# Performance work log

Hardware: AMD Instinct MI355X
Metric: run time of the kernel (lower is better)

Reference implementation:

```python
import jax, jax.numpy as jnp
import numpy as np

S, B, V, E, H, C, NV = 256, 64, 50000, 300, 512, 46, 4
EPS = 1e-8


def setup_inputs() -> dict:
    key = jax.random.key(0)
    ks = jax.random.split(key, 17)
    f = lambda i, shape, s=0.05: jax.random.normal(ks[i], shape, jnp.float32) * s
    return {
        "seq": jax.random.randint(ks[0], (S, B), 0, V),
        "emb_table": f(1, (V, E), 1.0),
        "w_ih0": f(2, (4 * H, E)), "w_hh0": f(3, (4 * H, H)),
        "b_ih0": f(4, (4 * H,)), "b_hh0": f(5, (4 * H,)),
        "w_ih1": f(6, (4 * H, H)), "w_hh1": f(7, (4 * H, H)),
        "b_ih1": f(8, (4 * H,)), "b_hh1": f(9, (4 * H,)),
        "lin_w": f(10, (H, H)), "lin_b": f(11, (H,)),
        "out_w": f(12, (C, H)), "out_b": f(13, (C,)),
        "pred_w": f(14, (C, 2 * C)), "pred_b": f(15, (C,)),
        "label_embed": f(16, (C, NV, E), 1.0),
    }


def _lstm_layer(x, w_ih, w_hh, b_ih, b_hh):
    # x: [S, B, in]; PyTorch gate order i, f, g, o
    bsz, hid = x.shape[1], w_hh.shape[1]

    def step(carry, xt):
        h, c = carry
        g = xt @ w_ih.T + h @ w_hh.T + b_ih + b_hh  # [B, 4H]
        i, fg, gg, o = jnp.split(g, 4, axis=-1)
        c = jax.nn.sigmoid(fg) * c + jax.nn.sigmoid(i) * jnp.tanh(gg)
        h = jax.nn.sigmoid(o) * jnp.tanh(c)
        return (h, c), h

    h0 = jnp.zeros((bsz, hid), x.dtype)
    _, hs = jax.lax.scan(step, (h0, h0), x)
    return hs  # [S, B, H]


def reference(seq, emb_table, w_ih0, w_hh0, b_ih0, b_hh0, w_ih1, w_hh1, b_ih1, b_hh1,
              lin_w, lin_b, out_w, out_b, pred_w, pred_b, label_embed):
    embed = emb_table[seq]  # [S, B, E]
    h = _lstm_layer(embed, w_ih0, w_hh0, b_ih0, b_hh0)
    h = _lstm_layer(h, w_ih1, w_hh1, b_ih1, b_hh1)  # dropout inactive (eval)
    feature = h[-1] @ lin_w.T + lin_b               # [B, H]
    lstm_output = feature @ out_w.T + out_b         # [B, C]

    # Batched replacement of the per-label/value cosine-similarity loop:
    # cos[s,b,c,v] = <embed[s,b], label[c,v]> / max(|embed[s,b]|*|label[c,v]|, eps)
    en = jnp.linalg.norm(embed, axis=-1)            # [S, B]
    ln = jnp.linalg.norm(label_embed, axis=-1)      # [C, V]
    num = jnp.einsum('sbe,cve->sbcv', embed, label_embed)
    cos = num / jnp.maximum(en[:, :, None, None] * ln[None, None, :, :], EPS)
    match_input = cos.max(axis=(0, 3))              # max over seq then values -> [B, C]

    x = jnp.concatenate([match_input, lstm_output], axis=1)  # [B, 2C]
    return x @ pred_w.T + pred_b                    # [B, C]
```

## Files before the change

kernel.cpp:

```cpp
#include <hip/hip_runtime.h>
#include <hip/hip_bf16.h>
#include <hip/hip_fp16.h>
#include <math.h>

#define S_LEN 256
#define BATCH 64
#define EMB 300
#define HID 512
#define NCLS 46
#define NVAL 4
#define G4H 2048
#define KPAD 320
#define NPADC 256
#define EPSV 1e-8f

using half8   = __attribute__((ext_vector_type(8))) _Float16;
using floatx4 = __attribute__((ext_vector_type(4))) float;

__device__ __forceinline__ float fsigm(float x) { return 1.f / (1.f + __expf(-x)); }
__device__ __forceinline__ float ftanh(float x) {
    float e2 = __expf(-2.f * x);
    return (1.f - e2) / (1.f + e2);
}
__device__ __forceinline__ float h2f(unsigned short u) {
    union { unsigned short s; _Float16 h; } cv; cv.s = u; return (float)cv.h;
}
__device__ __forceinline__ half8 pack8(const float* p) {
    float4 f0 = *(const float4*)p;
    float4 f1 = *(const float4*)(p + 4);
    half8 h;
    h[0] = (_Float16)f0.x; h[1] = (_Float16)f0.y; h[2] = (_Float16)f0.z; h[3] = (_Float16)f0.w;
    h[4] = (_Float16)f1.x; h[5] = (_Float16)f1.y; h[6] = (_Float16)f1.z; h[7] = (_Float16)f1.w;
    return h;
}

__global__ void k_label_norm(const float* __restrict__ label, float* __restrict__ ln) {
    int r = blockIdx.x;
    int lane = threadIdx.x;
    const float* row = label + (size_t)r * EMB;
    float ss = 0.f;
    for (int e = lane; e < EMB; e += 64) { float v = row[e]; ss += v * v; }
    #pragma unroll
    for (int off = 32; off; off >>= 1) ss += __shfl_down(ss, off);
    if (lane == 0) ln[r] = sqrtf(ss);
}

__global__ __launch_bounds__(256) void k_gather(const int* __restrict__ seq,
                                                const float* __restrict__ emb,
                                                float* __restrict__ embed,
                                                float* __restrict__ en) {
    int p = blockIdx.x * 4 + (threadIdx.x >> 6);
    int lane = threadIdx.x & 63;
    int row = seq[p];
    const float4* src = (const float4*)(emb + (size_t)row * EMB);
    float4* dst = (float4*)(embed + (size_t)p * EMB);
    float ss = 0.f;
    for (int e = lane; e < EMB / 4; e += 64) {
        float4 v = src[e];
        dst[e] = v;
        ss += v.x * v.x + v.y * v.y + v.z * v.z + v.w * v.w;
    }
    #pragma unroll
    for (int off = 32; off; off >>= 1) ss += __shfl_down(ss, off);
    if (lane == 0) en[p] = sqrtf(ss);
}

__global__ __launch_bounds__(256) void k_cvt(const float* __restrict__ in,
                                             unsigned short* __restrict__ out,
                                             int in_rows, int out_rows) {
    int r = blockIdx.x * 4 + (threadIdx.x >> 6);
    if (r >= out_rows) return;
    int lane = threadIdx.x & 63;
    for (int e = lane; e < 80; e += 64) {
        int c = e * 4;
        ushort4 o = {0, 0, 0, 0};
        if (r < in_rows && c < EMB) {
            float4 v = *(const float4*)(in + (size_t)r * EMB + c);
            union { _Float16 h; unsigned short s; } a, b, cc, d;
            a.h = (_Float16)v.x; b.h = (_Float16)v.y; cc.h = (_Float16)v.z; d.h = (_Float16)v.w;
            o.x = a.s; o.y = b.s; o.z = cc.s; o.w = d.s;
        }
        *(ushort4*)(out + (size_t)r * KPAD + c) = o;
    }
}

__global__ __launch_bounds__(256) void k_mkxh(const float* __restrict__ embed,
                                              unsigned short* __restrict__ Xh) {
    int p = blockIdx.x * 4 + (threadIdx.x >> 6);
    int lane = threadIdx.x & 63;
    const float4* src = (const float4*)(embed + (size_t)p * EMB);
    for (int e = lane; e < 80; e += 64) {
        ushort4 o = {0, 0, 0, 0};
        if (e < 75) {
            float4 v = src[e];
            union { _Float16 h; unsigned short s; } a, b, cc, d;
            a.h = (_Float16)v.x; b.h = (_Float16)v.y; cc.h = (_Float16)v.z; d.h = (_Float16)v.w;
            o.x = a.s; o.y = b.s; o.z = cc.s; o.w = d.s;
        }
        *(ushort4*)(Xh + (size_t)p * KPAD + e * 4) = o;
    }
}

template<int OUTF16>
__global__ __launch_bounds__(256) void k_gmm(const unsigned short* __restrict__ X,
                                             const unsigned short* __restrict__ W,
                                             const float* __restrict__ b1,
                                             const float* __restrict__ b2,
                                             void* __restrict__ Yv,
                                             int M, int N) {
    __shared__ __align__(16) char smem[20480];
    unsigned short (*Xs)[40] = (unsigned short(*)[40])smem;
    unsigned short (*Ws)[40] = (unsigned short(*)[40])(smem + 10240);

    int n0 = blockIdx.x * 128, m0 = blockIdx.y * 128;
    int tid = threadIdx.x;
    int w8 = tid >> 6, l = tid & 63, lj = l & 15, q8 = l >> 4;
    int wm = w8 & 1, wn = w8 >> 1;

    floatx4 acc[4][4];
    #pragma unroll
    for (int i = 0; i < 4; i++)
        #pragma unroll
        for (int j = 0; j < 4; j++) acc[i][j] = {0.f, 0.f, 0.f, 0.f};

    for (int k0 = 0; k0 < KPAD; k0 += 32) {
        #pragma unroll
        for (int i = 0; i < 2; i++) {
            int id = i * 256 + tid;
            int r = id >> 2, kc = (id & 3) * 8;
            *(uint4*)&Xs[r][kc] = *(const uint4*)&X[(size_t)(m0 + r) * KPAD + k0 + kc];
            *(uint4*)&Ws[r][kc] = *(const uint4*)&W[(size_t)(n0 + r) * KPAD + k0 + kc];
        }
        __syncthreads();
        half8 A[4], B[4];
        #pragma unroll
        for (int i = 0; i < 4; i++) A[i] = *(const half8*)&Xs[wm * 64 + i * 16 + lj][q8 * 8];
        #pragma unroll
        for (int j = 0; j < 4; j++) B[j] = *(const half8*)&Ws[wn * 64 + j * 16 + lj][q8 * 8];
        #pragma unroll
        for (int i = 0; i < 4; i++)
            #pragma unroll
            for (int j = 0; j < 4; j++)
                acc[i][j] = __builtin_amdgcn_mfma_f32_16x16x32_f16(A[i], B[j], acc[i][j], 0, 0, 0);
        __syncthreads();
    }

    #pragma unroll
    for (int j = 0; j < 4; j++) {
        int col = n0 + wn * 64 + j * 16 + lj;
        float bsum = OUTF16 ? (b1[col] + b2[col]) : 0.f;
        #pragma unroll
        for (int i = 0; i < 4; i++) {
            int row = m0 + wm * 64 + i * 16 + q8 * 4;
            #pragma unroll
            for (int reg = 0; reg < 4; reg++) {
                float v = acc[i][j][reg] + bsum;
                if (OUTF16) {
                    union { _Float16 h; unsigned short s; } cv; cv.h = (_Float16)v;
                    ((unsigned short*)Yv)[(size_t)(row + reg) * N + col] = cv.s;
                } else {
                    ((float*)Yv)[(size_t)(row + reg) * N + col] = v;
                }
            }
        }
    }
}

__global__ __launch_bounds__(256) void k_match(const float* __restrict__ num,
                                               const float* __restrict__ en,
                                               const float* __restrict__ ln,
                                               float* __restrict__ match) {
    int c = blockIdx.x, b = blockIdx.y;
    __shared__ float red[256];
    int s = threadIdx.x;
    float4 nv = *(const float4*)&num[((size_t)s * BATCH + b) * NPADC + c * 4];
    float enb = en[s * BATCH + b];
    float l0 = ln[c * 4 + 0], l1 = ln[c * 4 + 1], l2 = ln[c * 4 + 2], l3 = ln[c * 4 + 3];
    float m = nv.x / fmaxf(enb * l0, EPSV);
    m = fmaxf(m, nv.y / fmaxf(enb * l1, EPSV));
    m = fmaxf(m, nv.z / fmaxf(enb * l2, EPSV));
    m = fmaxf(m, nv.w / fmaxf(enb * l3, EPSV));
    red[s] = m;
    __syncthreads();
    for (int st = 128; st; st >>= 1) {
        if (s < st) red[s] = fmaxf(red[s], red[s + st]);
        __syncthreads();
    }
    if (s == 0) match[b * NCLS + c] = red[0];
}

__global__ __launch_bounds__(512) void k_lstm_pipe(
    const float* __restrict__ w_hh0,
    const unsigned short* __restrict__ G0,
    const float* __restrict__ w_ih1,
    const float* __restrict__ w_hh1,
    const float* __restrict__ b_ih1,
    const float* __restrict__ b_hh1,
    unsigned short* __restrict__ ring0,
    unsigned short* __restrict__ ring1,
    float* __restrict__ hlast,
    int* __restrict__ flags0,
    int* __restrict__ flags1)
{
    __shared__ __align__(16) char smem_raw[24576];
    int bid = blockIdx.x;
    int g = bid & 7;
    int tid = threadIdx.x;
    int w8 = tid >> 6, l = tid & 63, lj = l & 15, q8 = l >> 4;

    if (bid < 64) {
        int r = bid >> 3;
        _Float16 (*hl)[520] = (_Float16(*)[520])smem_raw;
        float (*gbuf)[260] = (float(*)[260])(smem_raw + 8320);

        half8 B0[16], B1[16];
        {
            int lc0 = w8 * 32 + lj;
            int lc1 = w8 * 32 + 16 + lj;
            int wr0 = (lc0 >> 6) * 512 + r * 64 + (lc0 & 63);
            int wr1 = (lc1 >> 6) * 512 + r * 64 + (lc1 & 63);
            #pragma unroll
            for (int kk = 0; kk < 16; kk++) {
                B0[kk] = pack8(w_hh0 + (size_t)wr0 * 512 + kk * 32 + q8 * 8);
                B1[kk] = pack8(w_hh0 + (size_t)wr1 * 512 + kk * 32 + q8 * 8);
            }
        }
        int gb_ = tid >> 6, gj = tid & 63;
        float cst = 0.f;

        for (int t = 0; t < S_LEN; t++) {
            const unsigned short* Gp = G0 + ((size_t)t * BATCH + g * 8 + gb_) * G4H + r * 64 + gj;
            float gv0 = h2f(Gp[0]), gv1 = h2f(Gp[512]), gv2 = h2f(Gp[1024]), gv3 = h2f(Gp[1536]);

            floatx4 acc0 = {0.f, 0.f, 0.f, 0.f}, acc1 = {0.f, 0.f, 0.f, 0.f};
            if (t > 0) {
                if (tid < 8) {
                    int gd = 1 << 20;
                    while (__hip_atomic_load(flags0 + g * 8 + tid, __ATOMIC_RELAXED,
                                             __HIP_MEMORY_SCOPE_AGENT) < t && --gd)
                        __builtin_amdgcn_s_sleep(1);
                }
                __syncthreads();
                {
                    int sb = tid >> 6, sk = (tid & 63) * 8;
                    const unsigned long long* src = (const unsigned long long*)
                        (ring0 + ((size_t)(t - 1) * BATCH + g * 8 + sb) * HID + sk);
                    unsigned long long v0 = __hip_atomic_load(src,     __ATOMIC_RELAXED, __HIP_MEMORY_SCOPE_AGENT);
                    unsigned long long v1 = __hip_atomic_load(src + 1, __ATOMIC_RELAXED, __HIP_MEMORY_SCOPE_AGENT);
                    *(unsigned long long*)&hl[sb][sk]     = v0;
                    *(unsigned long long*)&hl[sb][sk + 4] = v1;
                }
                __syncthreads();
                #pragma unroll
                for (int kk = 0; kk < 16; kk++) {
                    half8 A = *(const half8*)&hl[l & 7][kk * 32 + q8 * 8];
                    acc0 = __builtin_amdgcn_mfma_f32_16x16x32_f16(A, B0[kk], acc0, 0, 0, 0);
                    acc1 = __builtin_amdgcn_mfma_f32_16x16x32_f16(A, B1[kk], acc1, 0, 0, 0);
                }
                if (l < 32) {
                    #pragma unroll
                    for (int ri = 0; ri < 4; ri++) {
                        int row = q8 * 4 + ri;
                        gbuf[row][w8 * 32 + lj]      = acc0[ri];
                        gbuf[row][w8 * 32 + 16 + lj] = acc1[ri];
                    }
                }
                __syncthreads();
            }

            float s_i = gv0 + (t ? gbuf[gb_][gj]       : 0.f);
            float s_f = gv1 + (t ? gbuf[gb_][64 + gj]  : 0.f);
            float s_g = gv2 + (t ? gbuf[gb_][128 + gj] : 0.f);
            float s_o = gv3 + (t ? gbuf[gb_][192 + gj] : 0.f);
            cst = fsigm(s_f) * cst + fsigm(s_i) * ftanh(s_g);
            float hv = fsigm(s_o) * ftanh(cst);

            union { unsigned short s; _Float16 h; } cv; cv.h = (_Float16)hv;
            unsigned int mine = cv.s;
            unsigned int other = (unsigned int)__shfl_xor((int)mine, 1);
            if (!(gj & 1)) {
                unsigned int pk = (mine & 0xFFFFu) | (other << 16);
                unsigned int* rp = (unsigned int*)ring0;
                __hip_atomic_store(rp + (((size_t)t * BATCH + g * 8 + gb_) * HID + r * 64 + gj) / 2,
                                   pk, __ATOMIC_RELAXED, __HIP_MEMORY_SCOPE_AGENT);
            }
            __syncthreads();
            if (tid == 0)
                __hip_atomic_store(flags0 + g * 8 + r, t + 1, __ATOMIC_RELAXED, __HIP_MEMORY_SCOPE_AGENT);
        }
    } else {
        int rid = (bid - 64) >> 3;
        _Float16 (*hl0)[520] = (_Float16(*)[520])smem_raw;
        _Float16 (*hl1)[520] = (_Float16(*)[520])(smem_raw + 8320);
        float (*gbuf)[132] = (float(*)[132])(smem_raw + 16640);

        half8 Bin[16], Brec[16];
        {
            int gate = w8 >> 1;
            int wrow = gate * 512 + rid * 32 + (w8 & 1) * 16 + lj;
            #pragma unroll
            for (int kk = 0; kk < 16; kk++) {
                Bin[kk]  = pack8(w_ih1 + (size_t)wrow * 512 + kk * 32 + q8 * 8);
                Brec[kk] = pack8(w_hh1 + (size_t)wrow * 512 + kk * 32 + q8 * 8);
            }
        }
        float bi = 0.f, bf = 0.f, bgg = 0.f, bo = 0.f;
        if (tid < 256) {
            int u = tid & 31;
            int base = rid * 32 + u;
            bi  = b_ih1[base]        + b_hh1[base];
            bf  = b_ih1[512 + base]  + b_hh1[512 + base];
            bgg = b_ih1[1024 + base] + b_hh1[1024 + base];
            bo  = b_ih1[1536 + base] + b_hh1[1536 + base];
        }
        float cst = 0.f;

        for (int t = 0; t < S_LEN; t++) {
            if (tid < 8) {
                int gd = 1 << 20;
                while (__hip_atomic_load(flags0 + g * 8 + tid, __ATOMIC_RELAXED,
                                         __HIP_MEMORY_SCOPE_AGENT) < t + 1 && --gd)
                    __builtin_amdgcn_s_sleep(1);
            } else if (tid < 24 && t > 0) {
                int gd = 1 << 20;
                while (__hip_atomic_load(flags1 + g * 16 + (tid - 8), __ATOMIC_RELAXED,
                                         __HIP_MEMORY_SCOPE_AGENT) < t && --gd)
                    __builtin_amdgcn_s_sleep(1);
            }
            __syncthreads();

            {
                int sb = tid >> 6, sk = (tid & 63) * 8;
                const unsigned long long* s0 = (const unsigned long long*)
                    (ring0 + ((size_t)t * BATCH + g * 8 + sb) * HID + sk);
                unsigned long long v0 = __hip_atomic_load(s0,     __ATOMIC_RELAXED, __HIP_MEMORY_SCOPE_AGENT);
                unsigned long long v1 = __hip_atomic_load(s0 + 1, __ATOMIC_RELAXED, __HIP_MEMORY_SCOPE_AGENT);
                *(unsigned long long*)&hl0[sb][sk]     = v0;
                *(unsigned long long*)&hl0[sb][sk + 4] = v1;
                if (t > 0) {
                    const unsigned long long* s1 = (const unsigned long long*)
                        (ring1 + ((size_t)(t - 1) * BATCH + g * 8 + sb) * HID + sk);
                    unsigned long long u0 = __hip_atomic_load(s1,     __ATOMIC_RELAXED, __HIP_MEMORY_SCOPE_AGENT);
                    unsigned long long u1 = __hip_atomic_load(s1 + 1, __ATOMIC_RELAXED, __HIP_MEMORY_SCOPE_AGENT);
                    *(unsigned long long*)&hl1[sb][sk]     = u0;
                    *(unsigned long long*)&hl1[sb][sk + 4] = u1;
                }
            }
            __syncthreads();

            floatx4 accA = {0.f, 0.f, 0.f, 0.f}, accB = {0.f, 0.f, 0.f, 0.f};
            #pragma unroll
            for (int kk = 0; kk < 16; kk++) {
                half8 A0 = *(const half8*)&hl0[l & 7][kk * 32 + q8 * 8];
                accA = __builtin_amdgcn_mfma_f32_16x16x32_f16(A0, Bin[kk], accA, 0, 0, 0);
            }
            if (t > 0) {
                #pragma unroll
                for (int kk = 0; kk < 16; kk++) {
                    half8 A1 = *(const half8*)&hl1[l & 7][kk * 32 + q8 * 8];
                    accB = __builtin_amdgcn_mfma_f32_16x16x32_f16(A1, Brec[kk], accB, 0, 0, 0);
                }
            }
            if (l < 32) {
                #pragma unroll
                for (int ri = 0; ri < 4; ri++) {
                    int row = q8 * 4 + ri;
                    gbuf[row][w8 * 16 + lj] = accA[ri] + accB[ri];
                }
            }
            __syncthreads();

            if (tid < 256) {
                int b = tid >> 5, u = tid & 31;
                float s_i = gbuf[b][u]      + bi;
                float s_f = gbuf[b][32 + u] + bf;
                float s_g = gbuf[b][64 + u] + bgg;
                float s_o = gbuf[b][96 + u] + bo;
                cst = fsigm(s_f) * cst + fsigm(s_i) * ftanh(s_g);
                float hv = fsigm(s_o) * ftanh(cst);

                union { unsigned short s; _Float16 h; } cv; cv.h = (_Float16)hv;
                unsigned int mine = cv.s;
                unsigned int other = (unsigned int)__shfl_xor((int)mine, 1);
                if (!(u & 1)) {
                    unsigned int pk = (mine & 0xFFFFu) | (other << 16);
                    unsigned int* rp = (unsigned int*)ring1;
                    __hip_atomic_store(rp + (((size_t)t * BATCH + g * 8 + b) * HID + rid * 32 + u) / 2,
                                       pk, __ATOMIC_RELAXED, __HIP_MEMORY_SCOPE_AGENT);
                }
                if (t == S_LEN - 1)
                    hlast[(g * 8 + b) * HID + rid * 32 + u] = hv;
            }
            __syncthreads();
            if (tid == 0)
                __hip_atomic_store(flags1 + g * 16 + rid, t + 1, __ATOMIC_RELAXED, __HIP_MEMORY_SCOPE_AGENT);
        }
    }
}

__global__ void k_small(const float* __restrict__ X, const float* __restrict__ W,
                        const float* __restrict__ bias, float* __restrict__ Y,
                        int N, int K) {
    int m = blockIdx.x;
    int n = blockIdx.y * 64 + threadIdx.x;
    if (n >= N) return;
    const float* x = X + (size_t)m * K;
    const float* w = W + (size_t)n * K;
    float s = bias[n];
    for (int k = 0; k < K; k++) s += x[k] * w[k];
    Y[(size_t)m * N + n] = s;
}

__global__ void k_final(const float* __restrict__ match, const float* __restrict__ lout,
                        const float* __restrict__ W, const float* __restrict__ bias,
                        float* __restrict__ out) {
    int m = blockIdx.x;
    int n = threadIdx.x;
    if (n >= NCLS) return;
    const float* w = W + (size_t)n * (2 * NCLS);
    float s = bias[n];
    for (int k = 0; k < NCLS; k++) s += match[m * NCLS + k] * w[k];
    for (int k = 0; k < NCLS; k++) s += lout[m * NCLS + k] * w[NCLS + k];
    out[m * NCLS + n] = s;
}

extern "C" void kernel_launch(void* const* d_in, const int* in_sizes, int n_in,
                              void* d_out, int out_size, void* d_ws, size_t ws_size,
                              hipStream_t stream) {
    (void)in_sizes; (void)n_in; (void)out_size; (void)ws_size;
    const int*   seq    = (const int*)d_in[0];
    const float* emb    = (const float*)d_in[1];
    const float* w_ih0  = (const float*)d_in[2];
    const float* w_hh0  = (const float*)d_in[3];
    const float* b_ih0  = (const float*)d_in[4];
    const float* b_hh0  = (const float*)d_in[5];
    const float* w_ih1  = (const float*)d_in[6];
    const float* w_hh1  = (const float*)d_in[7];
    const float* b_ih1  = (const float*)d_in[8];
    const float* b_hh1  = (const float*)d_in[9];
    const float* lin_w  = (const float*)d_in[10];
    const float* lin_b  = (const float*)d_in[11];
    const float* out_w  = (const float*)d_in[12];
    const float* out_b  = (const float*)d_in[13];
    const float* pred_w = (const float*)d_in[14];
    const float* pred_b = (const float*)d_in[15];
    const float* label  = (const float*)d_in[16];

    const int M = S_LEN * BATCH;
    float* ws = (float*)d_ws;
    size_t o = 0;
    float* embed = ws + o; o += (size_t)M * EMB;
    unsigned short* G0 = (unsigned short*)(ws + o); o += (size_t)M * G4H / 2;
    unsigned short* ring0 = (unsigned short*)(ws + o); o += (size_t)M * HID / 2;
    unsigned short* ring1 = (unsigned short*)(ws + o); o += (size_t)M * HID / 2;
    float* h1last = ws + o; o += (size_t)BATCH * HID;
    float* en    = ws + o; o += M;
    float* ln    = ws + o; o += 256;
    float* match = ws + o; o += 3072;
    float* feat  = ws + o; o += (size_t)BATCH * HID;
    float* lout  = ws + o; o += 3072;
    int*   flags0 = (int*)(ws + o); o += 64;
    int*   flags1 = (int*)(ws + o); o += 128;
    unsigned short* Xh  = (unsigned short*)(ws + o); o += (size_t)M * KPAD / 2;
    unsigned short* Lh  = (unsigned short*)(ws + o); o += (size_t)NPADC * KPAD / 2;
    unsigned short* Wh0 = (unsigned short*)(ws + o); o += (size_t)G4H * KPAD / 2;
    float* numG  = ws + o; o += (size_t)M * NPADC;

    hipMemsetAsync(flags0, 0, 192 * sizeof(int), stream);

    k_label_norm<<<NCLS * NVAL, 64, 0, stream>>>(label, ln);
    k_gather<<<M / 4, 256, 0, stream>>>(seq, emb, embed, en);

    k_cvt<<<64, 256, 0, stream>>>(label, Lh, NCLS * NVAL, NPADC);
    k_cvt<<<512, 256, 0, stream>>>(w_ih0, Wh0, G4H, G4H);
    k_mkxh<<<M / 4, 256, 0, stream>>>(embed, Xh);

    k_gmm<0><<<dim3(NPADC / 128, M / 128), 256, 0, stream>>>(Xh, Lh, nullptr, nullptr, numG, M, NPADC);
    k_match<<<dim3(NCLS, BATCH), 256, 0, stream>>>(numG, en, ln, match);

    k_gmm<1><<<dim3(G4H / 128, M / 128), 256, 0, stream>>>(Xh, Wh0, b_ih0, b_hh0, G0, M, G4H);

    k_lstm_pipe<<<192, 512, 0, stream>>>(w_hh0, G0, w_ih1, w_hh1, b_ih1, b_hh1,
                                         ring0, ring1, h1last, flags0, flags1);

    k_small<<<dim3(BATCH, HID / 64), 64, 0, stream>>>(h1last, lin_w, lin_b, feat, HID, HID);
    k_small<<<dim3(BATCH, 1), 64, 0, stream>>>(feat, out_w, out_b, lout, NCLS, HID);
    k_final<<<BATCH, 64, 0, stream>>>(match, lout, pred_w, pred_b, (float*)d_out);
}
```

Baseline: 1.003 ms.

## Fuse preprocessing kernels and merge the two input GEMMs into one launch

Label norm and fp16 conversion now run in one kernel. The embedding gather writes fp16 Xh directly instead of staging fp32 embed and converting in a second pass. The cosine GEMM and layer-0 input GEMM are combined into a single grid that selects the weight matrix and output type by block column. This cuts launches and fp32 intermediate traffic, and lets the small cosine GEMM overlap with the larger one, at the cost of a uniform branch in the GEMM epilogue. The function-local extern declaration of k_cvtw is unusual but should compile.

```diff
diff --git a/kernel.cpp b/kernel.cpp
--- a/kernel.cpp
+++ b/kernel.cpp
@@ -34,85 +34,77 @@
     return h;
 }
 
-__global__ void k_label_norm(const float* __restrict__ label, float* __restrict__ ln) {
+__global__ void k_lab(const float* __restrict__ label, float* __restrict__ ln,
+                      unsigned short* __restrict__ Lh) {
     int r = blockIdx.x;
     int lane = threadIdx.x;
-    const float* row = label + (size_t)r * EMB;
     float ss = 0.f;
-    for (int e = lane; e < EMB; e += 64) { float v = row[e]; ss += v * v; }
-    #pragma unroll
-    for (int off = 32; off; off >>= 1) ss += __shfl_down(ss, off);
-    if (lane == 0) ln[r] = sqrtf(ss);
+    if (r < NCLS * NVAL) {
+        const float* row = label + (size_t)r * EMB;
+        for (int e = lane; e < 80; e += 64) {
+            ushort4 o = {0, 0, 0, 0};
+            if (e < 75) {
+                float4 v = *(const float4*)(row + e * 4);
+                ss += v.x * v.x + v.y * v.y + v.z * v.z + v.w * v.w;
+                union { _Float16 h; unsigned short s; } a, b, cc, d;
+                a.h = (_Float16)v.x; b.h = (_Float16)v.y; cc.h = (_Float16)v.z; d.h = (_Float16)v.w;
+                o.x = a.s; o.y = b.s; o.z = cc.s; o.w = d.s;
+            }
+            *(ushort4*)(Lh + (size_t)r * KPAD + e * 4) = o;
+        }
+        #pragma unroll
+        for (int off = 32; off; off >>= 1) ss += __shfl_down(ss, off);
+        if (lane == 0) ln[r] = sqrtf(ss);
+    } else {
+        for (int e = lane; e < 80; e += 64) {
+            ushort4 o = {0, 0, 0, 0};
+            *(ushort4*)(Lh + (size_t)r * KPAD + e * 4) = o;
+        }
+    }
 }
 
 __global__ __launch_bounds__(256) void k_gather(const int* __restrict__ seq,
                                                 const float* __restrict__ emb,
-                                                float* __restrict__ embed,
+                                                unsigned short* __restrict__ Xh,
                                                 float* __restrict__ en) {
     int p = blockIdx.x * 4 + (threadIdx.x >> 6);
     int lane = threadIdx.x & 63;
     int row = seq[p];
     const float4* src = (const float4*)(emb + (size_t)row * EMB);
-    float4* dst = (float4*)(embed + (size_t)p * EMB);
     float ss = 0.f;
-    for (int e = lane; e < EMB / 4; e += 64) {
-        float4 v = src[e];
-        dst[e] = v;
-        ss += v.x * v.x + v.y * v.y + v.z * v.z + v.w * v.w;
-    }
-    #pragma unroll
-    for (int off = 32; off; off >>= 1) ss += __shfl_down(ss, off);
-    if (lane == 0) en[p] = sqrtf(ss);
-}
-
-__global__ __launch_bounds__(256) void k_cvt(const float* __restrict__ in,
-                                             unsigned short* __restrict__ out,
-                                             int in_rows, int out_rows) {
-    int r = blockIdx.x * 4 + (threadIdx.x >> 6);
-    if (r >= out_rows) return;
-    int lane = threadIdx.x & 63;
-    for (int e = lane; e < 80; e += 64) {
-        int c = e * 4;
-        ushort4 o = {0, 0, 0, 0};
-        if (r < in_rows && c < EMB) {
-            float4 v = *(const float4*)(in + (size_t)r * EMB + c);
-            union { _Float16 h; unsigned short s; } a, b, cc, d;
-            a.h = (_Float16)v.x; b.h = (_Float16)v.y; cc.h = (_Float16)v.z; d.h = (_Float16)v.w;
-            o.x = a.s; o.y = b.s; o.z = cc.s; o.w = d.s;
-        }
-        *(ushort4*)(out + (size_t)r * KPAD + c) = o;
-    }
-}
-
-__global__ __launch_bounds__(256) void k_mkxh(const float* __restrict__ embed,
-                                              unsigned short* __restrict__ Xh) {
-    int p = blockIdx.x * 4 + (threadIdx.x >> 6);
-    int lane = threadIdx.x & 63;
-    const float4* src = (const float4*)(embed + (size_t)p * EMB);
     for (int e = lane; e < 80; e += 64) {
         ushort4 o = {0, 0, 0, 0};
         if (e < 75) {
             float4 v = src[e];
+            ss += v.x * v.x + v.y * v.y + v.z * v.z + v.w * v.w;
             union { _Float16 h; unsigned short s; } a, b, cc, d;
             a.h = (_Float16)v.x; b.h = (_Float16)v.y; cc.h = (_Float16)v.z; d.h = (_Float16)v.w;
             o.x = a.s; o.y = b.s; o.z = cc.s; o.w = d.s;
         }
         *(ushort4*)(Xh + (size_t)p * KPAD + e * 4) = o;
     }
-}
-
-template<int OUTF16>
-__global__ __launch_bounds__(256) void k_gmm(const unsigned short* __restrict__ X,
-                                             const unsigned short* __restrict__ W,
-                                             const float* __restrict__ b1,
-                                             const float* __restrict__ b2,
-                                             void* __restrict__ Yv,
-                                             int M, int N) {
+    #pragma unroll
+    for (int off = 32; off; off >>= 1) ss += __shfl_down(ss, off);
+    if (lane == 0) en[p] = sqrtf(ss);
+}
+
+__global__ __launch_bounds__(256) void k_gmm_all(const unsigned short* __restrict__ X,
+                                                 const unsigned short* __restrict__ Wh0,
+                                                 const unsigned short* __restrict__ Lh,
+                                                 const float* __restrict__ b1,
+                                                 const float* __restrict__ b2,
+                                                 unsigned short* __restrict__ G0,
+                                                 float* __restrict__ numG) {
     __shared__ __align__(16) char smem[20480];
     unsigned short (*Xs)[40] = (unsigned short(*)[40])smem;
     unsigned short (*Ws)[40] = (unsigned short(*)[40])(smem + 10240);
 
-    int n0 = blockIdx.x * 128, m0 = blockIdx.y * 128;
+    int bx = blockIdx.x;
+    bool iscos = bx >= 16;
+    const unsigned short* W = iscos ? Lh : Wh0;
+    int N = iscos ? NPADC : G4H;
+    int n0 = (iscos ? bx - 16 : bx) * 128;
+    int m0 = blockIdx.y * 128;
     int tid = threadIdx.x;
     int w8 = tid >> 6, l = tid & 63, lj = l & 15, q8 = l >> 4;
     int wm = w8 & 1, wn = w8 >> 1;
@@ -148,18 +140,18 @@
     #pragma unroll
     for (int j = 0; j < 4; j++) {
         int col = n0 + wn * 64 + j * 16 + lj;
-        float bsum = OUTF16 ? (b1[col] + b2[col]) : 0.f;
+        float bsum = iscos ? 0.f : (b1[col] + b2[col]);
         #pragma unroll
         for (int i = 0; i < 4; i++) {
             int row = m0 + wm * 64 + i * 16 + q8 * 4;
             #pragma unroll
             for (int reg = 0; reg < 4; reg++) {
                 float v = acc[i][j][reg] + bsum;
-                if (OUTF16) {
+                if (iscos) {
+                    numG[(size_t)(row + reg) * NPADC + col] = v;
+                } else {
                     union { _Float16 h; unsigned short s; } cv; cv.h = (_Float16)v;
-                    ((unsigned short*)Yv)[(size_t)(row + reg) * N + col] = cv.s;
-                } else {
-                    ((float*)Yv)[(size_t)(row + reg) * N + col] = v;
+                    G0[(size_t)(row + reg) * G4H + col] = cv.s;
                 }
             }
         }
@@ -449,7 +441,6 @@
     const int M = S_LEN * BATCH;
     float* ws = (float*)d_ws;
     size_t o = 0;
-    float* embed = ws + o; o += (size_t)M * EMB;
     unsigned short* G0 = (unsigned short*)(ws + o); o += (size_t)M * G4H / 2;
     unsigned short* ring0 = (unsigned short*)(ws + o); o += (size_t)M * HID / 2;
     unsigned short* ring1 = (unsigned short*)(ws + o); o += (size_t)M * HID / 2;
@@ -468,17 +459,16 @@
 
     hipMemsetAsync(flags0, 0, 192 * sizeof(int), stream);
 
-    k_label_norm<<<NCLS * NVAL, 64, 0, stream>>>(label, ln);
-    k_gather<<<M / 4, 256, 0, stream>>>(seq, emb, embed, en);
-
-    k_cvt<<<64, 256, 0, stream>>>(label, Lh, NCLS * NVAL, NPADC);
-    k_cvt<<<512, 256, 0, stream>>>(w_ih0, Wh0, G4H, G4H);
-    k_mkxh<<<M / 4, 256, 0, stream>>>(embed, Xh);
-
-    k_gmm<0><<<dim3(NPADC / 128, M / 128), 256, 0, stream>>>(Xh, Lh, nullptr, nullptr, numG, M, NPADC);
+    k_lab<<<NPADC, 64, 0, stream>>>(label, ln, Lh);
+    k_gather<<<M / 4, 256, 0, stream>>>(seq, emb, Xh, en);
+    {
+    }
+    struct _dummy {};
+    extern __global__ void k_cvtw(const float*, unsigned short*);
+    k_cvtw<<<512, 256, 0, stream>>>(w_ih0, Wh0);
+
+    k_gmm_all<<<dim3(18, M / 128), 256, 0, stream>>>(Xh, Wh0, Lh, b_ih0, b_hh0, G0, numG);
     k_match<<<dim3(NCLS, BATCH), 256, 0, stream>>>(numG, en, ln, match);
-
-    k_gmm<1><<<dim3(G4H / 128, M / 128), 256, 0, stream>>>(Xh, Wh0, b_ih0, b_hh0, G0, M, G4H);
 
     k_lstm_pipe<<<192, 512, 0, stream>>>(w_hh0, G0, w_ih1, w_hh1, b_ih1, b_hh1,
                                          ring0, ring1, h1last, flags0, flags1);
@@ -487,3 +477,20 @@
     k_small<<<dim3(BATCH, 1), 64, 0, stream>>>(feat, out_w, out_b, lout, NCLS, HID);
     k_final<<<BATCH, 64, 0, stream>>>(match, lout, pred_w, pred_b, (float*)d_out);
 }
+
+__global__ __launch_bounds__(256) void k_cvtw(const float* __restrict__ in,
+                                              unsigned short* __restrict__ out) {
+    int r = blockIdx.x * 4 + (threadIdx.x >> 6);
+    int lane = threadIdx.x & 63;
+    for (int e = lane; e < 80; e += 64) {
+        int c = e * 4;
+        ushort4 o = {0, 0, 0, 0};
+        if (c < EMB) {
+            float4 v = *(const float4*)(in + (size_t)r * EMB + c);
+            union { _Float16 h; unsigned short s; } a, b, cc, d;
+            a.h = (_Float16)v.x; b.h = (_Float16)v.y; cc.h = (_Float16)v.z; d.h = (_Float16)v.w;
+            o.x = a.s; o.y = b.s; o.z = cc.s; o.w = d.s;
+        }
+        *(ushort4*)(out + (size_t)r * KPAD + c) = o;
+    }
+}
```

Result: no change. 987.0 us (-1.6%).
